# Kernel optimization log

Measured on AMD Instinct MI355X. Metric: run time of the kernel, lower is better.

## Reference

```python
import jax, jax.numpy as jnp
import numpy as np


def setup_inputs() -> dict:
    key = jax.random.key(0)
    B, C, N = 1, 8, 320
    n_shots, spp = 4, 1502
    inp = jax.random.normal(key, (B, C, N, N, 2), dtype=jnp.float32)
    # radial trajectory initialization, faithful to initilaize_trajectory('radial')
    theta = np.pi / n_shots
    L = np.arange(-160, 160, 320.0 / spp, dtype=np.float32)[:spp]
    traj = np.zeros((n_shots, spp, 2), dtype=np.float32)
    for i in range(n_shots):
        traj[i, :, 0] = L * np.cos(theta * i)
        traj[i, :, 1] = L * np.sin(theta * i)
    return {"inp": inp, "traj": jnp.asarray(traj)}


def _nufft_roundtrip(inp, traj):
    # inp: [B, C, H, W, 2] real/imag pairs; traj: [n_shots, spp, 2] in [-N/2, N/2)
    N = inp.shape[2]
    img = (inp[..., 0] + 1j * inp[..., 1]).astype(jnp.complex64)  # [B,C,H,W]
    xf = traj.reshape(-1, 2)                                      # [M,2]
    kx, ky = xf[:, 0], xf[:, 1]
    grid = (jnp.arange(N) - N // 2).astype(jnp.float32)           # centered pixel coords
    w = jnp.complex64(-2j * jnp.pi / N)
    Ax = jnp.exp(w * (kx[:, None] * grid[None, :])).astype(jnp.complex64)  # [M,H]
    Ay = jnp.exp(w * (ky[:, None] * grid[None, :])).astype(jnp.complex64)  # [M,W]
    # type-2 NUFFT (exact nonuniform DFT): image -> nonuniform k-space samples
    t = jnp.einsum('mx,bcxy->bcmy', Ax, img)        # [B,C,M,W]
    ksp = jnp.einsum('bcmy,my->bcm', t, Ay)         # [B,C,M]
    # adjoint (type-1): nonuniform samples -> Cartesian image grid
    tmp = ksp[..., None] * jnp.conj(Ay)[None, None]  # [B,C,M,W]
    out = jnp.einsum('mx,bcmw->bcxw', jnp.conj(Ax), tmp)  # [B,C,H,W]
    return jnp.stack([out.real, out.imag], axis=-1)  # [B,C,H,W,2]


def reference(inp, traj):
    return _nufft_roundtrip(inp, traj)
```

## Files before the change

### kernel.cpp

```cpp
#include <hip/hip_runtime.h>
#include <math.h>


#define NN      320
#define BCC     8
#define MREAL   6008
#define MSTR    6144
#define MT1     47
#define P1STR   6016
#define SKADJ   8
#define CHUNKM  (MSTR / SKADJ)
#define NADJB   (SKADJ * BCC * 25)
#define TWOPI   6.283185307179586f

typedef __attribute__((ext_vector_type(8))) short short8_t;
typedef __attribute__((ext_vector_type(4))) float float4_t;

__device__ __forceinline__ unsigned short f2bf(float f) {
    union { float f; unsigned u; } v; v.f = f;
    unsigned r = v.u + 0x7fff + ((v.u >> 16) & 1);
    return (unsigned short)(r >> 16);
}
__device__ __forceinline__ float bf2f(unsigned short h) {
    union { unsigned u; float f; } v; v.u = ((unsigned)h) << 16;
    return v.f;
}
__device__ __forceinline__ short8_t neg8(short8_t v) {
    short8_t r;
    #pragma unroll
    for (int i = 0; i < 8; ++i) r[i] = v[i] ^ (short)0x8000;
    return r;
}
__device__ __forceinline__ float gval(int i) { return (float)(i - NN/2); }

__device__ __forceinline__ void phase_cs(float k, float g, float* c, float* s) {
    float rev = k * (g * (1.0f / (float)NN));
    rev -= rintf(rev);
    float th = rev * TWOPI;
    __sincosf(th, s, c);
}

__device__ __forceinline__ void gld16(const unsigned short* g, unsigned short* l) {
    __builtin_amdgcn_global_load_lds(
        (const __attribute__((address_space(1))) unsigned int*)g,
        (__attribute__((address_space(3))) unsigned int*)l, 16, 0, 0);
}

__global__ __launch_bounds__(256) void gen_A(
    const float* __restrict__ traj,
    unsigned short* __restrict__ Ax_r, unsigned short* __restrict__ Ax_i,
    unsigned short* __restrict__ AxT_r, unsigned short* __restrict__ AxT_i,
    unsigned short* __restrict__ AyT_r, unsigned short* __restrict__ AyT_i)
{
    __shared__ __align__(16) float lc[64][65];
    __shared__ __align__(16) float ls[64][65];
    __shared__ float kxv[64], kyv[64];
    const int tid = threadIdx.x;
    const int m0 = blockIdx.x * 64;
    const int g0 = blockIdx.y * 64;

    if (tid < 64) {
        int m = m0 + tid;
        kxv[tid] = (m < MREAL) ? traj[2*m]     : 0.f;
        kyv[tid] = (m < MREAL) ? traj[2*m + 1] : 0.f;
    }
    __syncthreads();

    #pragma unroll
    for (int it = 0; it < 16; ++it) {
        int e = tid + it * 256;
        int mi = e >> 6, gi = e & 63;
        float c, s;
        phase_cs(kxv[mi], gval(g0 + gi), &c, &s);
        bool valid = (m0 + mi) < MREAL;
        lc[mi][gi] = valid ? c : 0.f;
        ls[mi][gi] = valid ? s : 0.f;
    }
    __syncthreads();
    #pragma unroll
    for (int it = 0; it < 16; ++it) {
        int e = tid + it * 256;
        int mi = e >> 6, xi = e & 63;
        int m = m0 + mi;
        size_t o = (size_t)m * NN + g0 + (xi ^ ((m & 7) << 3));
        Ax_r[o] = f2bf(lc[mi][xi]);
        Ax_i[o] = f2bf(-ls[mi][xi]);
    }
    #pragma unroll
    for (int it = 0; it < 16; ++it) {
        int e = tid + it * 256;
        int xi = e >> 6, mi = e & 63;
        int x = g0 + xi;
        size_t o = (size_t)x * MSTR + m0 + (mi ^ ((x & 7) << 3));
        AxT_r[o] = f2bf(lc[mi][xi]);
        AxT_i[o] = f2bf(ls[mi][xi]);
    }
    __syncthreads();

    #pragma unroll
    for (int it = 0; it < 16; ++it) {
        int e = tid + it * 256;
        int mi = e >> 6, gi = e & 63;
        float c, s;
        phase_cs(kyv[mi], gval(g0 + gi), &c, &s);
        bool valid = (m0 + mi) < MREAL;
        lc[mi][gi] = valid ? c : 0.f;
        ls[mi][gi] = valid ? s : 0.f;
    }
    __syncthreads();
    #pragma unroll
    for (int it = 0; it < 16; ++it) {
        int e = tid + it * 256;
        int yi = e >> 6, mi = e & 63;
        size_t o = (size_t)(g0 + yi) * MSTR + (m0 + mi);
        AyT_r[o] = f2bf(lc[mi][yi]);
        AyT_i[o] = f2bf(ls[mi][yi]);
    }
}

__global__ __launch_bounds__(256) void conv_img(
    const float* __restrict__ inp,
    unsigned short* __restrict__ iT_r, unsigned short* __restrict__ iT_i)
{
    __shared__ __align__(16) float2 t[64][65];
    const int tid = threadIdx.x;
    const int x0 = blockIdx.x * 64, y0 = blockIdx.y * 64, bc = blockIdx.z;
    const float2* ip = (const float2*)inp;
    #pragma unroll
    for (int it = 0; it < 16; ++it) {
        int e = tid + it * 256;
        int r = e >> 6, c = e & 63;
        t[r][c] = ip[((size_t)bc * NN + (x0 + r)) * NN + (y0 + c)];
    }
    __syncthreads();
    #pragma unroll
    for (int it = 0; it < 16; ++it) {
        int e = tid + it * 256;
        int yy = e >> 6, xx = e & 63;
        float2 v = t[xx][yy];
        int y = y0 + yy;
        size_t o = ((size_t)bc * NN + y) * NN + x0 + (xx ^ ((y & 7) << 3));
        iT_r[o] = f2bf(v.x);
        iT_i[o] = f2bf(v.y);
    }
}

__device__ __forceinline__ void fcompute(
    const unsigned short* ST, float4_t (&accR)[2][4], float4_t (&accI)[2][4],
    int kb, int sxor, int wy, int wm, int ar)
{
    #pragma unroll
    for (int ks = 0; ks < 2; ++ks) {
        const int e = (ks * 32 + kb * 8) ^ sxor;
        short8_t a_r[2], a_i[2], a_n[2], b_r[4], b_i[4];
        #pragma unroll
        for (int iy = 0; iy < 2; ++iy) {
            int rr = wy * 32 + iy * 16 + ar;
            a_r[iy] = *(const short8_t*)&ST[rr * 64 + e];
            a_i[iy] = *(const short8_t*)&ST[4096 + rr * 64 + e];
            a_n[iy] = neg8(a_i[iy]);
        }
        #pragma unroll
        for (int jm = 0; jm < 4; ++jm) {
            int cc = wm * 64 + jm * 16 + ar;
            b_r[jm] = *(const short8_t*)&ST[8192  + cc * 64 + e];
            b_i[jm] = *(const short8_t*)&ST[16384 + cc * 64 + e];
        }
        #pragma unroll
        for (int iy = 0; iy < 2; ++iy)
            #pragma unroll
            for (int jm = 0; jm < 4; ++jm) {
                accR[iy][jm] = __builtin_amdgcn_mfma_f32_16x16x32_bf16(a_r[iy], b_r[jm], accR[iy][jm], 0, 0, 0);
                accR[iy][jm] = __builtin_amdgcn_mfma_f32_16x16x32_bf16(a_n[iy], b_i[jm], accR[iy][jm], 0, 0, 0);
                accI[iy][jm] = __builtin_amdgcn_mfma_f32_16x16x32_bf16(a_r[iy], b_i[jm], accI[iy][jm], 0, 0, 0);
                accI[iy][jm] = __builtin_amdgcn_mfma_f32_16x16x32_bf16(a_i[iy], b_r[jm], accI[iy][jm], 0, 0, 0);
            }
    }
}

__global__ __launch_bounds__(256) void fwd_gemm(
    const unsigned short* __restrict__ iT_r, const unsigned short* __restrict__ iT_i,
    const unsigned short* __restrict__ Ax_r, const unsigned short* __restrict__ Ax_i,
    const unsigned short* __restrict__ AyT_r, const unsigned short* __restrict__ AyT_i,
    float2* __restrict__ partial1)
{
    __shared__ __align__(16) unsigned short ST[24576];
    __shared__ __align__(16) float2 redbuf[2][128];

    const int tid = threadIdx.x;
    const int bid = blockIdx.x;
    const int nid = (bid & 7) * 235 + (bid >> 3);
    const int mt  = nid / 40;
    const int r40 = nid - mt * 40;
    const int yt  = r40 % 5;
    const int bc  = r40 / 5;
    const int m0  = mt * 128;
    const int y0  = yt * 64;

    float4_t accR[2][4], accI[2][4];
    #pragma unroll
    for (int i = 0; i < 2; ++i)
        #pragma unroll
        for (int j = 0; j < 4; ++j) { accR[i][j] = (float4_t)0.f; accI[i][j] = (float4_t)0.f; }

    const int lane = tid & 63, wid = tid >> 6;
    const int wy = wid & 1, wm = wid >> 1;
    const int ar = lane & 15, kb = lane >> 4;
    const int sxor = (lane & 7) << 3;

    const int lrow = lane >> 3;
    const int cb8  = (lane & 7) * 8;

    const unsigned short* gp[12];
    unsigned short* lp[12];
    #pragma unroll
    for (int j = 0; j < 12; ++j) {
        int s = wid + 4 * j;
        const unsigned short* g;
        if (s < 16) {
            int row = (s & 7) * 8 + lrow;
            const unsigned short* pl = (s < 8) ? iT_r : iT_i;
            g = pl + ((size_t)bc * NN + (y0 + row)) * NN + cb8;
        } else {
            int row = ((s - 16) & 15) * 8 + lrow;
            const unsigned short* pl = (s < 32) ? Ax_r : Ax_i;
            g = pl + (size_t)(m0 + row) * NN + cb8;
        }
        gp[j] = g;
        lp[j] = &ST[s * 512];
    }

    for (int t = 0; t < 5; ++t) {
        #pragma unroll
        for (int j = 0; j < 12; ++j) gld16(gp[j], lp[j]);
        #pragma unroll
        for (int j = 0; j < 12; ++j) gp[j] += 64;
        __syncthreads();
        fcompute(&ST[0], accR, accI, kb, sxor, wy, wm, ar);
        __syncthreads();
    }

    #pragma unroll
    for (int jm = 0; jm < 4; ++jm) {
        float sr = 0.f, si = 0.f;
        int m = m0 + wm * 64 + jm * 16 + ar;
        #pragma unroll
        for (int iy = 0; iy < 2; ++iy)
            #pragma unroll
            for (int q = 0; q < 4; ++q) {
                int y = y0 + wy * 32 + iy * 16 + kb * 4 + q;
                float c  = bf2f(AyT_r[(size_t)y * MSTR + m]);
                float sy = bf2f(AyT_i[(size_t)y * MSTR + m]);
                float Tr = accR[iy][jm][q], Ti = accI[iy][jm][q];
                sr += Tr * c + Ti * sy;
                si += Ti * c - Tr * sy;
            }
        sr += __shfl_xor(sr, 16); sr += __shfl_xor(sr, 32);
        si += __shfl_xor(si, 16); si += __shfl_xor(si, 32);
        if ((lane & 48) == 0)
            redbuf[wy][wm * 64 + jm * 16 + ar] = make_float2(sr, si);
    }
    __syncthreads();
    if (tid < 128) {
        float2 a = redbuf[0][tid], b = redbuf[1][tid];
        int m = m0 + tid;
        if (m < MREAL)
            partial1[((size_t)bc * 5 + yt) * P1STR + m] = make_float2(a.x + b.x, a.y + b.y);
    }
}

__global__ void reduce_ksp(const float2* __restrict__ partial1,
                           float2* __restrict__ ksp)
{
    int mp = blockIdx.x * 256 + threadIdx.x;
    int bc = blockIdx.y;
    float2 r = make_float2(0.f, 0.f);
    if (mp < MREAL) {
        #pragma unroll
        for (int yt = 0; yt < 5; ++yt) {
            float2 v = partial1[((size_t)bc * 5 + yt) * P1STR + mp];
            r.x += v.x; r.y += v.y;
        }
    }
    ksp[(size_t)bc * MSTR + mp] = r;
}

__global__ __launch_bounds__(256) void gen_U(
    const unsigned short* __restrict__ AyT_r, const unsigned short* __restrict__ AyT_i,
    const float2* __restrict__ ksp,
    unsigned short* __restrict__ U_r, unsigned short* __restrict__ U_i)
{
    const int tid = threadIdx.x;
    const int m0 = blockIdx.x * 2048 + tid * 8;
    const int y  = blockIdx.y;
    const int bc = blockIdx.z;

    short8_t yr = *(const short8_t*)(AyT_r + (size_t)y * MSTR + m0);
    short8_t yi = *(const short8_t*)(AyT_i + (size_t)y * MSTR + m0);
    const float2* kp = ksp + (size_t)bc * MSTR + m0;
    short8_t ur, ui;
    #pragma unroll
    for (int j = 0; j < 8; ++j) {
        float2 k = kp[j];
        float cr = bf2f((unsigned short)yr[j]);
        float ci = bf2f((unsigned short)yi[j]);
        ur[j] = (short)f2bf(k.x * cr - k.y * ci);
        ui[j] = (short)f2bf(k.x * ci + k.y * cr);
    }
    size_t o = ((size_t)bc * NN + y) * MSTR + (m0 ^ ((y & 7) << 3));
    *(short8_t*)(U_r + o) = ur;
    *(short8_t*)(U_i + o) = ui;
}

__device__ __forceinline__ void acompute(
    const unsigned short* ST, float4_t (&accR)[2][2], float4_t (&accI)[2][2],
    int kb, int sxor, int wx, int wyy, int ar)
{
    #pragma unroll
    for (int ks = 0; ks < 2; ++ks) {
        const int e = (ks * 32 + kb * 8) ^ sxor;
        short8_t a_r[2], a_i[2], a_n[2], b_r[2], b_i[2];
        #pragma unroll
        for (int ix = 0; ix < 2; ++ix) {
            int rr = wx * 32 + ix * 16 + ar;
            a_r[ix] = *(const short8_t*)&ST[rr * 64 + e];
            a_i[ix] = *(const short8_t*)&ST[4096 + rr * 64 + e];
            a_n[ix] = neg8(a_i[ix]);
        }
        #pragma unroll
        for (int jy = 0; jy < 2; ++jy) {
            int cc = wyy * 32 + jy * 16 + ar;
            b_r[jy] = *(const short8_t*)&ST[8192  + cc * 64 + e];
            b_i[jy] = *(const short8_t*)&ST[12288 + cc * 64 + e];
        }
        #pragma unroll
        for (int ix = 0; ix < 2; ++ix)
            #pragma unroll
            for (int jy = 0; jy < 2; ++jy) {
                accR[ix][jy] = __builtin_amdgcn_mfma_f32_16x16x32_bf16(a_r[ix], b_r[jy], accR[ix][jy], 0, 0, 0);
                accR[ix][jy] = __builtin_amdgcn_mfma_f32_16x16x32_bf16(a_n[ix], b_i[jy], accR[ix][jy], 0, 0, 0);
                accI[ix][jy] = __builtin_amdgcn_mfma_f32_16x16x32_bf16(a_r[ix], b_i[jy], accI[ix][jy], 0, 0, 0);
                accI[ix][jy] = __builtin_amdgcn_mfma_f32_16x16x32_bf16(a_i[ix], b_r[jy], accI[ix][jy], 0, 0, 0);
            }
    }
}

template<int FP32P>
__global__ __launch_bounds__(256) void adj_gemm_pre(
    const unsigned short* __restrict__ AxT_r, const unsigned short* __restrict__ AxT_i,
    const unsigned short* __restrict__ U_r, const unsigned short* __restrict__ U_i,
    void* __restrict__ partial2)
{
    __shared__ __align__(16) unsigned short ST[16384];

    const int tid = threadIdx.x;
    const int bid = blockIdx.x;
    const int nid = (bid & 7) * (NADJB / 8) + (bid >> 3);
    const int bcsk = nid / 25;
    const int xy = nid - bcsk * 25;
    const int xt = xy / 5, yt = xy % 5;
    const int bc = bcsk % BCC, sk = bcsk / BCC;
    const int x0 = xt * 64, y0 = yt * 64;
    const int kbeg = sk * CHUNKM;

    float4_t accR[2][2], accI[2][2];
    #pragma unroll
    for (int i = 0; i < 2; ++i)
        #pragma unroll
        for (int j = 0; j < 2; ++j) { accR[i][j] = (float4_t)0.f; accI[i][j] = (float4_t)0.f; }

    const int lane = tid & 63, wid = tid >> 6;
    const int wx = wid >> 1, wyy = wid & 1;
    const int ar = lane & 15, kb = lane >> 4;
    const int sxor = (lane & 7) << 3;

    const int lrow = lane >> 3;
    const int cb8  = (lane & 7) * 8;

    const unsigned short* gp[8];
    unsigned short* lp[8];
    #pragma unroll
    for (int j = 0; j < 8; ++j) {
        int s = wid + 4 * j;
        int row = (s & 7) * 8 + lrow;
        const unsigned short* g;
        if (s < 16) {
            const unsigned short* pl = (s < 8) ? AxT_r : AxT_i;
            g = pl + (size_t)(x0 + row) * MSTR + kbeg + cb8;
        } else {
            const unsigned short* pl = (s < 24) ? U_r : U_i;
            g = pl + ((size_t)bc * NN + (y0 + row)) * MSTR + kbeg + cb8;
        }
        gp[j] = g;
        lp[j] = &ST[s * 512];
    }

    for (int t = 0; t < CHUNKM / 64; ++t) {
        #pragma unroll
        for (int j = 0; j < 8; ++j) gld16(gp[j], lp[j]);
        #pragma unroll
        for (int j = 0; j < 8; ++j) gp[j] += 64;
        __syncthreads();
        acompute(&ST[0], accR, accI, kb, sxor, wx, wyy, ar);
        __syncthreads();
    }

    #pragma unroll
    for (int ix = 0; ix < 2; ++ix)
        #pragma unroll
        for (int jy = 0; jy < 2; ++jy)
            #pragma unroll
            for (int q = 0; q < 4; ++q) {
                int x = x0 + wx * 32 + ix * 16 + kb * 4 + q;
                int y = y0 + wyy * 32 + jy * 16 + ar;
                size_t o = (((size_t)sk * BCC + bc) * NN + x) * NN + y;
                float vr = accR[ix][jy][q], vi = accI[ix][jy][q];
                if (FP32P) {
                    ((float2*)partial2)[o] = make_float2(vr, vi);
                } else {
                    ((unsigned*)partial2)[o] =
                        (unsigned)f2bf(vr) | ((unsigned)f2bf(vi) << 16);
                }
            }
}

template<int FP32P>
__global__ __launch_bounds__(256) void adj_gemm_fb(
    const unsigned short* __restrict__ AxT_r, const unsigned short* __restrict__ AxT_i,
    const unsigned short* __restrict__ AyT_r, const unsigned short* __restrict__ AyT_i,
    const float2* __restrict__ ksp, void* __restrict__ partial2)
{
    __shared__ __align__(16) unsigned short Ar[64][72], Ai[64][72];
    __shared__ __align__(16) unsigned short Br[64][72], Bi[64][72];
    __shared__ __align__(16) float2 kspl[CHUNKM];

    const int tid = threadIdx.x;
    const int bid = blockIdx.x;
    const int nid = (bid & 7) * (NADJB / 8) + (bid >> 3);
    const int bcsk = nid / 25;
    const int xy = nid - bcsk * 25;
    const int xt = xy / 5, yt = xy % 5;
    const int bc = bcsk % BCC, sk = bcsk / BCC;
    const int x0 = xt * 64, y0 = yt * 64;
    const int kbeg = sk * CHUNKM;

    #pragma unroll
    for (int it = 0; it < CHUNKM / 256; ++it)
        kspl[tid + it * 256] = ksp[(size_t)bc * MSTR + kbeg + tid + it * 256];
    __syncthreads();

    float4_t accR[2][2], accI[2][2];
    #pragma unroll
    for (int i = 0; i < 2; ++i)
        #pragma unroll
        for (int j = 0; j < 2; ++j) { accR[i][j] = (float4_t)0.f; accI[i][j] = (float4_t)0.f; }

    const int lane = tid & 63, wid = tid >> 6;
    const int wx = wid >> 1, wyy = wid & 1;
    const int ar = lane & 15, kb = lane >> 4;
    const int sxor = (lane & 7) << 3;

    for (int mk = 0; mk < CHUNKM; mk += 64) {
        #pragma unroll
        for (int it = 0; it < 2; ++it) {
            int e = tid + it * 256;
            int row = e >> 3, gr = e & 7;
            size_t o = (size_t)(x0 + row) * MSTR + kbeg + mk + gr * 8;
            *(short8_t*)&Ar[row][gr * 8] = *(const short8_t*)(AxT_r + o);
            *(short8_t*)&Ai[row][gr * 8] = *(const short8_t*)(AxT_i + o);
        }
        #pragma unroll
        for (int it = 0; it < 2; ++it) {
            int e = tid + it * 256;
            int row = e >> 3, gr = e & 7;
            size_t o = (size_t)(y0 + row) * MSTR + kbeg + mk + gr * 8;
            short8_t yr = *(const short8_t*)(AyT_r + o);
            short8_t yi = *(const short8_t*)(AyT_i + o);
            short8_t br, bi2;
            #pragma unroll
            for (int j = 0; j < 8; ++j) {
                float2 k = kspl[mk + gr * 8 + j];
                float cr = bf2f((unsigned short)yr[j]);
                float ci = bf2f((unsigned short)yi[j]);
                br[j]  = (short)f2bf(k.x * cr - k.y * ci);
                bi2[j] = (short)f2bf(k.x * ci + k.y * cr);
            }
            *(short8_t*)&Br[row][gr * 8] = br;
            *(short8_t*)&Bi[row][gr * 8] = bi2;
        }
        __syncthreads();

        #pragma unroll
        for (int ks = 0; ks < 2; ++ks) {
            const int ea = (ks * 32 + kb * 8) ^ sxor;
            const int eb = ks * 32 + kb * 8;
            short8_t a_r[2], a_i[2], a_n[2], b_r[2], b_i[2];
            #pragma unroll
            for (int ix = 0; ix < 2; ++ix) {
                int rr = wx * 32 + ix * 16 + ar;
                a_r[ix] = *(const short8_t*)&Ar[rr][ea];
                a_i[ix] = *(const short8_t*)&Ai[rr][ea];
                a_n[ix] = neg8(a_i[ix]);
            }
            #pragma unroll
            for (int jy = 0; jy < 2; ++jy) {
                int cc = wyy * 32 + jy * 16 + ar;
                b_r[jy] = *(const short8_t*)&Br[cc][eb];
                b_i[jy] = *(const short8_t*)&Bi[cc][eb];
            }
            #pragma unroll
            for (int ix = 0; ix < 2; ++ix)
                #pragma unroll
                for (int jy = 0; jy < 2; ++jy) {
                    accR[ix][jy] = __builtin_amdgcn_mfma_f32_16x16x32_bf16(a_r[ix], b_r[jy], accR[ix][jy], 0, 0, 0);
                    accR[ix][jy] = __builtin_amdgcn_mfma_f32_16x16x32_bf16(a_n[ix], b_i[jy], accR[ix][jy], 0, 0, 0);
                    accI[ix][jy] = __builtin_amdgcn_mfma_f32_16x16x32_bf16(a_r[ix], b_i[jy], accI[ix][jy], 0, 0, 0);
                    accI[ix][jy] = __builtin_amdgcn_mfma_f32_16x16x32_bf16(a_i[ix], b_r[jy], accI[ix][jy], 0, 0, 0);
                }
        }
        __syncthreads();
    }

    #pragma unroll
    for (int ix = 0; ix < 2; ++ix)
        #pragma unroll
        for (int jy = 0; jy < 2; ++jy)
            #pragma unroll
            for (int q = 0; q < 4; ++q) {
                int x = x0 + wx * 32 + ix * 16 + kb * 4 + q;
                int y = y0 + wyy * 32 + jy * 16 + ar;
                size_t o = (((size_t)sk * BCC + bc) * NN + x) * NN + y;
                float vr = accR[ix][jy][q], vi = accI[ix][jy][q];
                if (FP32P) {
                    ((float2*)partial2)[o] = make_float2(vr, vi);
                } else {
                    ((unsigned*)partial2)[o] =
                        (unsigned)f2bf(vr) | ((unsigned)f2bf(vi) << 16);
                }
            }
}

template<int FP32P>
__global__ void reduce_out(const void* __restrict__ partial2,
                           float2* __restrict__ out)
{
    size_t total = (size_t)BCC * NN * NN;
    size_t idx = (size_t)blockIdx.x * 256 + threadIdx.x;
    if (idx >= total) return;
    float2 r = make_float2(0.f, 0.f);
    #pragma unroll
    for (int s = 0; s < SKADJ; ++s) {
        if (FP32P) {
            float2 v = ((const float2*)partial2)[s * total + idx];
            r.x += v.x; r.y += v.y;
        } else {
            unsigned u = ((const unsigned*)partial2)[s * total + idx];
            r.x += bf2f((unsigned short)(u & 0xffff));
            r.y += bf2f((unsigned short)(u >> 16));
        }
    }
    out[idx] = r;
}

extern "C" void kernel_launch(void* const* d_in, const int* in_sizes, int n_in,
                              void* d_out, int out_size, void* d_ws, size_t ws_size,
                              hipStream_t stream)
{
    const float* inp  = (const float*)d_in[0];
    const float* traj = (const float*)d_in[1];

    char* ws = (char*)d_ws;
    const size_t PL = (size_t)NN * MSTR * 2;
    unsigned short* AxT_r = (unsigned short*)(ws);
    unsigned short* AxT_i = (unsigned short*)(ws + PL);
    unsigned short* AyT_r = (unsigned short*)(ws + 2 * PL);
    unsigned short* AyT_i = (unsigned short*)(ws + 3 * PL);
    float2* ksp = (float2*)(ws + 4 * PL);
    const size_t KSPB = (size_t)BCC * MSTR * 8;
    const size_t BASE = 4 * PL + KSPB;
    char* rb = ws + BASE;
    unsigned short* Ax_r = (unsigned short*)(rb);
    unsigned short* Ax_i = (unsigned short*)(rb + PL);
    const size_t ITP = (size_t)BCC * NN * NN * 2;
    unsigned short* iT_r = (unsigned short*)(rb + 2 * PL);
    unsigned short* iT_i = (unsigned short*)(rb + 2 * PL + ITP);
    float2* partial1 = (float2*)(rb + 2 * PL + 2 * ITP);
    const size_t UPL = (size_t)BCC * NN * MSTR * 2;
    unsigned short* U_r = (unsigned short*)(rb);
    unsigned short* U_i = (unsigned short*)(rb + UPL);
    const size_t ADJ_F32 = (size_t)SKADJ * BCC * NN * NN * 8;
    const size_t ADJ_B16 = ADJ_F32 / 2;

    gen_A<<<dim3(96, 5), 256, 0, stream>>>(traj, Ax_r, Ax_i, AxT_r, AxT_i, AyT_r, AyT_i);
    conv_img<<<dim3(5, 5, BCC), 256, 0, stream>>>(inp, iT_r, iT_i);
    fwd_gemm<<<dim3(1880), 256, 0, stream>>>(iT_r, iT_i, Ax_r, Ax_i, AyT_r, AyT_i, partial1);
    reduce_ksp<<<dim3(24, BCC), 256, 0, stream>>>(partial1, ksp);

    size_t total = (size_t)BCC * NN * NN;
    int rblocks = (int)((total + 255) / 256);

    if (ws_size >= BASE + 2 * UPL + ADJ_B16) {
        void* partial2 = (void*)(rb + 2 * UPL);
        gen_U<<<dim3(3, NN, BCC), 256, 0, stream>>>(AyT_r, AyT_i, ksp, U_r, U_i);
        adj_gemm_pre<0><<<dim3(NADJB), 256, 0, stream>>>(AxT_r, AxT_i, U_r, U_i, partial2);
        reduce_out<0><<<rblocks, 256, 0, stream>>>(partial2, (float2*)d_out);
    } else if (ws_size >= BASE + ADJ_F32) {
        void* partial2 = (void*)rb;
        adj_gemm_fb<1><<<dim3(NADJB), 256, 0, stream>>>(AxT_r, AxT_i, AyT_r, AyT_i, ksp, partial2);
        reduce_out<1><<<rblocks, 256, 0, stream>>>(partial2, (float2*)d_out);
    } else {
        void* partial2 = (void*)rb;
        adj_gemm_fb<0><<<dim3(NADJB), 256, 0, stream>>>(AxT_r, AxT_i, AyT_r, AyT_i, ksp, partial2);
        reduce_out<0><<<rblocks, 256, 0, stream>>>(partial2, (float2*)d_out);
    }
}
```

Before: 132.0 us.

## Enlarge forward GEMM tile to 256 samples per block with full-height waves

The forward GEMM block tile grows from 128 to 256 trajectory samples, so each wave now covers all 64 image rows and its own 64-sample column slice. The shared-memory reduction across wave rows goes away and partial results are written straight to global memory. Shared memory grows to 80 KB, allocated dynamically, and the grid halves to 960 blocks. The aim is more reuse of the image tile per load and fewer redundant loads. In exchange, doubling the accumulators raises register pressure and the larger LDS footprint lowers occupancy.

```diff
diff --git a/kernel.cpp b/kernel.cpp
--- a/kernel.cpp
+++ b/kernel.cpp
@@ -6,7 +6,6 @@
 #define BCC     8
 #define MREAL   6008
 #define MSTR    6144
-#define MT1     47
 #define P1STR   6016
 #define SKADJ   8
 #define CHUNKM  (MSTR / SKADJ)
@@ -145,76 +144,41 @@
     }
 }
 
-__device__ __forceinline__ void fcompute(
-    const unsigned short* ST, float4_t (&accR)[2][4], float4_t (&accI)[2][4],
-    int kb, int sxor, int wy, int wm, int ar)
-{
-    #pragma unroll
-    for (int ks = 0; ks < 2; ++ks) {
-        const int e = (ks * 32 + kb * 8) ^ sxor;
-        short8_t a_r[2], a_i[2], a_n[2], b_r[4], b_i[4];
-        #pragma unroll
-        for (int iy = 0; iy < 2; ++iy) {
-            int rr = wy * 32 + iy * 16 + ar;
-            a_r[iy] = *(const short8_t*)&ST[rr * 64 + e];
-            a_i[iy] = *(const short8_t*)&ST[4096 + rr * 64 + e];
-            a_n[iy] = neg8(a_i[iy]);
-        }
-        #pragma unroll
-        for (int jm = 0; jm < 4; ++jm) {
-            int cc = wm * 64 + jm * 16 + ar;
-            b_r[jm] = *(const short8_t*)&ST[8192  + cc * 64 + e];
-            b_i[jm] = *(const short8_t*)&ST[16384 + cc * 64 + e];
-        }
-        #pragma unroll
-        for (int iy = 0; iy < 2; ++iy)
-            #pragma unroll
-            for (int jm = 0; jm < 4; ++jm) {
-                accR[iy][jm] = __builtin_amdgcn_mfma_f32_16x16x32_bf16(a_r[iy], b_r[jm], accR[iy][jm], 0, 0, 0);
-                accR[iy][jm] = __builtin_amdgcn_mfma_f32_16x16x32_bf16(a_n[iy], b_i[jm], accR[iy][jm], 0, 0, 0);
-                accI[iy][jm] = __builtin_amdgcn_mfma_f32_16x16x32_bf16(a_r[iy], b_i[jm], accI[iy][jm], 0, 0, 0);
-                accI[iy][jm] = __builtin_amdgcn_mfma_f32_16x16x32_bf16(a_i[iy], b_r[jm], accI[iy][jm], 0, 0, 0);
-            }
-    }
-}
-
 __global__ __launch_bounds__(256) void fwd_gemm(
     const unsigned short* __restrict__ iT_r, const unsigned short* __restrict__ iT_i,
     const unsigned short* __restrict__ Ax_r, const unsigned short* __restrict__ Ax_i,
     const unsigned short* __restrict__ AyT_r, const unsigned short* __restrict__ AyT_i,
     float2* __restrict__ partial1)
 {
-    __shared__ __align__(16) unsigned short ST[24576];
-    __shared__ __align__(16) float2 redbuf[2][128];
+    extern __shared__ __align__(16) unsigned short ST[];
 
     const int tid = threadIdx.x;
     const int bid = blockIdx.x;
-    const int nid = (bid & 7) * 235 + (bid >> 3);
+    const int nid = (bid & 7) * 120 + (bid >> 3);
     const int mt  = nid / 40;
     const int r40 = nid - mt * 40;
     const int yt  = r40 % 5;
     const int bc  = r40 / 5;
-    const int m0  = mt * 128;
+    const int m0  = mt * 256;
     const int y0  = yt * 64;
 
-    float4_t accR[2][4], accI[2][4];
-    #pragma unroll
-    for (int i = 0; i < 2; ++i)
+    float4_t accR[4][4], accI[4][4];
+    #pragma unroll
+    for (int i = 0; i < 4; ++i)
         #pragma unroll
         for (int j = 0; j < 4; ++j) { accR[i][j] = (float4_t)0.f; accI[i][j] = (float4_t)0.f; }
 
     const int lane = tid & 63, wid = tid >> 6;
-    const int wy = wid & 1, wm = wid >> 1;
     const int ar = lane & 15, kb = lane >> 4;
     const int sxor = (lane & 7) << 3;
 
     const int lrow = lane >> 3;
     const int cb8  = (lane & 7) * 8;
 
-    const unsigned short* gp[12];
-    unsigned short* lp[12];
-    #pragma unroll
-    for (int j = 0; j < 12; ++j) {
+    const unsigned short* gp[20];
+    unsigned short* lp[20];
+    #pragma unroll
+    for (int j = 0; j < 20; ++j) {
         int s = wid + 4 * j;
         const unsigned short* g;
         if (s < 16) {
@@ -222,8 +186,8 @@
             const unsigned short* pl = (s < 8) ? iT_r : iT_i;
             g = pl + ((size_t)bc * NN + (y0 + row)) * NN + cb8;
         } else {
-            int row = ((s - 16) & 15) * 8 + lrow;
-            const unsigned short* pl = (s < 32) ? Ax_r : Ax_i;
+            int row = ((s - 16) & 31) * 8 + lrow;
+            const unsigned short* pl = (s < 48) ? Ax_r : Ax_i;
             g = pl + (size_t)(m0 + row) * NN + cb8;
         }
         gp[j] = g;
@@ -232,23 +196,50 @@
 
     for (int t = 0; t < 5; ++t) {
         #pragma unroll
-        for (int j = 0; j < 12; ++j) gld16(gp[j], lp[j]);
-        #pragma unroll
-        for (int j = 0; j < 12; ++j) gp[j] += 64;
+        for (int j = 0; j < 20; ++j) gld16(gp[j], lp[j]);
+        #pragma unroll
+        for (int j = 0; j < 20; ++j) gp[j] += 64;
         __syncthreads();
-        fcompute(&ST[0], accR, accI, kb, sxor, wy, wm, ar);
+
+        #pragma unroll
+        for (int ks = 0; ks < 2; ++ks) {
+            const int e = (ks * 32 + kb * 8) ^ sxor;
+            short8_t a_r[4], a_i[4], a_n[4], b_r[4], b_i[4];
+            #pragma unroll
+            for (int iy = 0; iy < 4; ++iy) {
+                int rr = iy * 16 + ar;
+                a_r[iy] = *(const short8_t*)&ST[rr * 64 + e];
+                a_i[iy] = *(const short8_t*)&ST[4096 + rr * 64 + e];
+                a_n[iy] = neg8(a_i[iy]);
+            }
+            #pragma unroll
+            for (int jm = 0; jm < 4; ++jm) {
+                int cc = wid * 64 + jm * 16 + ar;
+                b_r[jm] = *(const short8_t*)&ST[8192  + cc * 64 + e];
+                b_i[jm] = *(const short8_t*)&ST[24576 + cc * 64 + e];
+            }
+            #pragma unroll
+            for (int iy = 0; iy < 4; ++iy)
+                #pragma unroll
+                for (int jm = 0; jm < 4; ++jm) {
+                    accR[iy][jm] = __builtin_amdgcn_mfma_f32_16x16x32_bf16(a_r[iy], b_r[jm], accR[iy][jm], 0, 0, 0);
+                    accR[iy][jm] = __builtin_amdgcn_mfma_f32_16x16x32_bf16(a_n[iy], b_i[jm], accR[iy][jm], 0, 0, 0);
+                    accI[iy][jm] = __builtin_amdgcn_mfma_f32_16x16x32_bf16(a_r[iy], b_i[jm], accI[iy][jm], 0, 0, 0);
+                    accI[iy][jm] = __builtin_amdgcn_mfma_f32_16x16x32_bf16(a_i[iy], b_r[jm], accI[iy][jm], 0, 0, 0);
+                }
+        }
         __syncthreads();
     }
 
     #pragma unroll
     for (int jm = 0; jm < 4; ++jm) {
         float sr = 0.f, si = 0.f;
-        int m = m0 + wm * 64 + jm * 16 + ar;
-        #pragma unroll
-        for (int iy = 0; iy < 2; ++iy)
+        int m = m0 + wid * 64 + jm * 16 + ar;
+        #pragma unroll
+        for (int iy = 0; iy < 4; ++iy)
             #pragma unroll
             for (int q = 0; q < 4; ++q) {
-                int y = y0 + wy * 32 + iy * 16 + kb * 4 + q;
+                int y = y0 + iy * 16 + kb * 4 + q;
                 float c  = bf2f(AyT_r[(size_t)y * MSTR + m]);
                 float sy = bf2f(AyT_i[(size_t)y * MSTR + m]);
                 float Tr = accR[iy][jm][q], Ti = accI[iy][jm][q];
@@ -257,15 +248,8 @@
             }
         sr += __shfl_xor(sr, 16); sr += __shfl_xor(sr, 32);
         si += __shfl_xor(si, 16); si += __shfl_xor(si, 32);
-        if ((lane & 48) == 0)
-            redbuf[wy][wm * 64 + jm * 16 + ar] = make_float2(sr, si);
-    }
-    __syncthreads();
-    if (tid < 128) {
-        float2 a = redbuf[0][tid], b = redbuf[1][tid];
-        int m = m0 + tid;
-        if (m < MREAL)
-            partial1[((size_t)bc * 5 + yt) * P1STR + m] = make_float2(a.x + b.x, a.y + b.y);
+        if ((lane & 48) == 0 && m < MREAL)
+            partial1[((size_t)bc * 5 + yt) * P1STR + m] = make_float2(sr, si);
     }
 }
 
@@ -593,7 +577,7 @@
 
     gen_A<<<dim3(96, 5), 256, 0, stream>>>(traj, Ax_r, Ax_i, AxT_r, AxT_i, AyT_r, AyT_i);
     conv_img<<<dim3(5, 5, BCC), 256, 0, stream>>>(inp, iT_r, iT_i);
-    fwd_gemm<<<dim3(1880), 256, 0, stream>>>(iT_r, iT_i, Ax_r, Ax_i, AyT_r, AyT_i, partial1);
+    fwd_gemm<<<dim3(960), 256, 81920, stream>>>(iT_r, iT_i, Ax_r, Ax_i, AyT_r, AyT_i, partial1);
     reduce_ksp<<<dim3(24, BCC), 256, 0, stream>>>(partial1, ksp);
 
     size_t total = (size_t)BCC * NN * NN;
```

Result: slower. 150.9 us (+14.4%).
